# Performance work log

Hardware: AMD Instinct MI355X
Metric: run time of the kernel (lower is better)

The kernel has to match this reference:

```python
import jax, jax.numpy as jnp
import numpy as np

H, D_MODEL, D_K, D_V = 16, 1024, 64, 64
B, L = 4, 2048

def _linear_params(key, in_dim, out_dim):
    kw, kb = jax.random.split(key)
    bound = 1.0 / np.sqrt(in_dim)
    W = jax.random.uniform(kw, (out_dim, in_dim), jnp.float32, -bound, bound)
    b = jax.random.uniform(kb, (out_dim,), jnp.float32, -bound, bound)
    return W, b

def setup_inputs() -> dict:
    key = jax.random.key(0)
    ks = jax.random.split(key, 7)
    V = jax.random.normal(ks[0], (B, L, D_MODEL), jnp.float32)
    K = jax.random.normal(ks[1], (B, L, D_MODEL), jnp.float32)
    Q = jax.random.normal(ks[2], (B, L, D_MODEL), jnp.float32)
    Wv, bv = _linear_params(ks[3], D_MODEL, H * D_V)
    Wk, bk = _linear_params(ks[4], D_MODEL, H * D_K)
    Wq, bq = _linear_params(ks[5], D_MODEL, H * D_K)
    Wo, bo = _linear_params(ks[6], H * D_V, D_MODEL)
    return {"V": V, "K": K, "Q": Q, "Wv": Wv, "bv": bv, "Wk": Wk, "bk": bk,
            "Wq": Wq, "bq": bq, "Wo": Wo, "bo": bo}

def reference(V, K, Q, Wv, bv, Wk, bk, Wq, bq, Wo, bo):
    batch, len1, _ = V.shape
    len2 = Q.shape[1]
    # project and split heads: (b, l, h, d)
    v = (V @ Wv.T + bv).reshape(batch, len1, H, D_V)
    k = (K @ Wk.T + bk).reshape(batch, len1, H, D_K)
    q = (Q @ Wq.T + bq).reshape(batch, len2, H, D_K)
    scale = 1.0 / jnp.sqrt(jnp.asarray(D_K, q.dtype))
    # scores: (b, h, len2, len1)
    scores = jnp.einsum('bqhd,bkhd->bhqk', q, k) * scale
    attn = jax.nn.softmax(scores, axis=-1)
    out = jnp.einsum('bhqk,bkhd->bqhd', attn, v).reshape(batch, len2, H * D_V)
    return out @ Wo.T + bo
```

## Files before the change

### kernel.cpp

```cpp
#include <hip/hip_runtime.h>


typedef __bf16 bf16;
typedef __attribute__((ext_vector_type(8))) __bf16 bf16x8;
typedef __attribute__((ext_vector_type(4))) __bf16 bf16x4;
typedef __attribute__((ext_vector_type(4))) float f32x4;
typedef __attribute__((ext_vector_type(16))) float f32x16;

__global__ __launch_bounds__(256) void cvt_all(
    const float* __restrict__ Q, const float* __restrict__ K, const float* __restrict__ V,
    const float* __restrict__ Wq, const float* __restrict__ Wk,
    const float* __restrict__ Wv, const float* __restrict__ Wo,
    bf16* __restrict__ ws)
{
    int bid = blockIdx.x;
    const float* src;
    bf16* dst;
    int lb;
    if (bid < 4096)       { src = Q;  dst = ws;             lb = bid; }
    else if (bid < 8192)  { src = K;  dst = ws + 8388608;   lb = bid - 4096; }
    else if (bid < 12288) { src = V;  dst = ws + 16777216;  lb = bid - 8192; }
    else if (bid < 12800) { src = Wq; dst = ws + 25165824;  lb = bid - 12288; }
    else if (bid < 13312) { src = Wk; dst = ws + 26214400;  lb = bid - 12800; }
    else if (bid < 13824) { src = Wv; dst = ws + 27262976;  lb = bid - 13312; }
    else                  { src = Wo; dst = ws + 28311552;  lb = bid - 13824; }
    size_t i = ((size_t)lb * 256 + threadIdx.x) * 8;
    f32x4 a = *(const f32x4*)(src + i);
    f32x4 b = *(const f32x4*)(src + i + 4);
    bf16x8 o;
    o[0] = (bf16)a[0]; o[1] = (bf16)a[1]; o[2] = (bf16)a[2]; o[3] = (bf16)a[3];
    o[4] = (bf16)b[0]; o[5] = (bf16)b[1]; o[6] = (bf16)b[2]; o[7] = (bf16)b[3];
    *(bf16x8*)(dst + i) = o;
}

__device__ inline void gld_lds16(const void* g, void* l) {
    __builtin_amdgcn_global_load_lds((const __attribute__((address_space(1))) void*)g,
                                     (__attribute__((address_space(3))) void*)l, 16, 0, 0);
}

__global__ __launch_bounds__(512, 2) void proj_fused(
    const bf16* __restrict__ Xq, const bf16* __restrict__ Xk, const bf16* __restrict__ Xv,
    const bf16* __restrict__ Wqb, const bf16* __restrict__ Wkb, const bf16* __restrict__ Wvb,
    const float* __restrict__ bq, const float* __restrict__ bk, const float* __restrict__ bv,
    bf16* __restrict__ qw, bf16* __restrict__ kw, bf16* __restrict__ vtw)
{
    __shared__ bf16 lA[3][8192];
    __shared__ bf16 lB[3][8192];

    const int bid = blockIdx.x;
    const int xcd = bid & 7, idx = bid >> 3;
    const int chunk = idx >> 3, within = idx & 7;
    const int gc = xcd * 6 + chunk;
    const int z  = gc >> 4;
    const int mp = gc & 15;
    const int m0 = (mp * 2 + (within >> 2)) * 256;
    const int n0 = (within & 3) * 256;

    const bf16*  A    = z == 0 ? Xq  : (z == 1 ? Xk  : Xv);
    const bf16*  W    = z == 0 ? Wqb : (z == 1 ? Wkb : Wvb);
    const float* bias = z == 0 ? bq  : (z == 1 ? bk  : bv);
    bf16*        out  = z == 0 ? qw  : (z == 1 ? kw  : vtw);
    const float scale = z == 0 ? 0.18033688011112042f : 1.0f;

    const int tid  = threadIdx.x;
    const int wave = tid >> 6, lane = tid & 63;
    const int c = lane & 15, g = lane >> 4;
    const int wm = wave >> 2, wn = wave & 3;

    const int srow = lane >> 2;
    const int scol = ((lane & 3) ^ ((lane >> 3) & 3)) * 8;
    const int rsw  = (g ^ ((c >> 1) & 3)) * 8;

    f32x4 acc[8][4] = {};

#define SA(kt_, bb)                                                             \
    {                                                                           \
        _Pragma("unroll")                                                       \
        for (int j = 0; j < 2; ++j)                                             \
            gld_lds16(A + (size_t)(m0 + j * 128 + wave * 16 + srow) * 1024 +    \
                          (kt_) * 32 + scol,                                    \
                      &lA[bb][j * 4096 + wave * 512]);                          \
    }
#define SB(kt_, bb)                                                             \
    {                                                                           \
        _Pragma("unroll")                                                       \
        for (int j = 0; j < 2; ++j)                                             \
            gld_lds16(W + (size_t)(n0 + j * 128 + wave * 16 + srow) * 1024 +    \
                          (kt_) * 32 + scol,                                    \
                      &lB[bb][j * 4096 + wave * 512]);                          \
    }

    SA(0, 0); SB(0, 0);
    SA(1, 1); SB(1, 1);

    int buf = 0;
    for (int u = 0; u < 32; ++u) {
        if (u < 31) {
            asm volatile("s_waitcnt vmcnt(4)" ::: "memory");
        } else {
            asm volatile("s_waitcnt vmcnt(0)" ::: "memory");
        }
        __builtin_amdgcn_s_barrier();
        asm volatile("" ::: "memory");

        bf16x8 af[8], bfr[4];
#pragma unroll
        for (int m = 0; m < 8; ++m)
            af[m] = *(const bf16x8*)&lA[buf][(wm * 128 + m * 16 + c) * 32 + rsw];
#pragma unroll
        for (int n = 0; n < 4; ++n)
            bfr[n] = *(const bf16x8*)&lB[buf][(wn * 64 + n * 16 + c) * 32 + rsw];

        if (u + 2 < 32) {
            int nb = buf + 2; if (nb >= 3) nb -= 3;
            SA(u + 2, nb); SB(u + 2, nb);
        }

#pragma unroll
        for (int m = 0; m < 8; ++m)
#pragma unroll
            for (int n = 0; n < 4; ++n)
                acc[m][n] = __builtin_amdgcn_mfma_f32_16x16x32_bf16(af[m], bfr[n], acc[m][n], 0, 0, 0);

        buf = (buf == 2) ? 0 : buf + 1;
    }
#undef SA
#undef SB

#pragma unroll
    for (int m = 0; m < 8; ++m) {
#pragma unroll
        for (int n = 0; n < 4; ++n) {
            int col  = n0 + wn * 64 + n * 16 + c;
            float bb = bias[col];
#pragma unroll
            for (int r = 0; r < 4; ++r) {
                int row = m0 + wm * 128 + m * 16 + 4 * g + r;
                float v = (acc[m][n][r] + bb) * scale;
                int b = row >> 11, l = row & 2047, hh = col >> 6, d = col & 63;
                size_t base = (size_t)(b * 16 + hh) * 131072;
                if (z < 2) {
                    out[base + (l >> 5) * 2048 + (d >> 4) * 512 +
                        ((d >> 3) & 1) * 256 + (l & 31) * 8 + (d & 7)] = (bf16)v;
                } else {
                    out[base + (l >> 5) * 2048 + (d >> 5) * 1024 +
                        ((l >> 4) & 1) * 512 + ((l >> 3) & 1) * 256 +
                        (d & 31) * 8 + (l & 7)] = (bf16)v;
                }
            }
        }
    }
}

__global__ __launch_bounds__(256) void gemm_out(
    const bf16* __restrict__ A, const bf16* __restrict__ W,
    const float* __restrict__ bias, float* __restrict__ out)
{
    __shared__ bf16 lA[2][8192];
    __shared__ bf16 lB[2][8192];
    const int tid  = threadIdx.x;
    const int wave = tid >> 6, lane = tid & 63;
    const int c = lane & 15, g = lane >> 4;

    const int oid = blockIdx.y * 8 + blockIdx.x;
    const int nid = (oid & 7) * 64 + (oid >> 3);
    const int m0 = (nid >> 3) * 128, n0 = (nid & 7) * 128;

    const int wr = wave >> 1, wc = wave & 1;
    const int srow  = lane >> 3;
    const int scol8 = ((lane & 7) ^ srow) * 8;
    const int c7 = c & 7;

    f32x4 acc[4][4] = {};

#define OSTAGE(kt_, bb)                                                         \
    {                                                                           \
        _Pragma("unroll")                                                       \
        for (int i = 0; i < 4; ++i) {                                           \
            int ca = wave * 4 + i;                                              \
            int arow = ca * 8 + srow;                                           \
            gld_lds16(A + (size_t)(m0 + arow) * 1024 + (kt_) * 64 + scol8,      \
                      &lA[bb][ca * 512]);                                       \
            gld_lds16(W + (size_t)(n0 + arow) * 1024 + (kt_) * 64 + scol8,      \
                      &lB[bb][ca * 512]);                                       \
        }                                                                       \
    }

    OSTAGE(0, 0);
    OSTAGE(1, 1);

    for (int kt = 0; kt < 16; ++kt) {
        const int buf = kt & 1;
        if (kt < 15) {
            asm volatile("s_waitcnt vmcnt(8)" ::: "memory");
        } else {
            asm volatile("s_waitcnt vmcnt(0)" ::: "memory");
        }
        __builtin_amdgcn_s_barrier();
        asm volatile("" ::: "memory");

#pragma unroll
        for (int ks = 0; ks < 2; ++ks) {
            bf16x8 af[4], bfr[4];
#pragma unroll
            for (int m = 0; m < 4; ++m) {
                int r = wr * 64 + m * 16 + c;
                af[m] = *(const bf16x8*)&lA[buf][r * 64 + (((ks * 4 + g) ^ c7) * 8)];
            }
#pragma unroll
            for (int n = 0; n < 4; ++n) {
                int r = wc * 64 + n * 16 + c;
                bfr[n] = *(const bf16x8*)&lB[buf][r * 64 + (((ks * 4 + g) ^ c7) * 8)];
            }
#pragma unroll
            for (int m = 0; m < 4; ++m)
#pragma unroll
                for (int n = 0; n < 4; ++n)
                    acc[m][n] = __builtin_amdgcn_mfma_f32_16x16x32_bf16(af[m], bfr[n], acc[m][n], 0, 0, 0);
        }

        asm volatile("" ::: "memory");
        __builtin_amdgcn_s_barrier();
        asm volatile("" ::: "memory");
        if (kt + 2 < 16) OSTAGE(kt + 2, buf);
    }
#undef OSTAGE

#pragma unroll
    for (int m = 0; m < 4; ++m) {
#pragma unroll
        for (int n = 0; n < 4; ++n) {
            int col  = n0 + wc * 64 + n * 16 + c;
            float bb = bias[col];
#pragma unroll
            for (int r = 0; r < 4; ++r) {
                int row = m0 + wr * 64 + m * 16 + 4 * g + r;
                out[(size_t)row * 1024 + col] = acc[m][n][r] + bb;
            }
        }
    }
}

__device__ inline unsigned cvtpk(float lo, float hi) {
    unsigned r;
    asm("v_cvt_pk_bf16_f32 %0, %1, %2" : "=v"(r) : "v"(lo), "v"(hi));
    return r;
}
__device__ inline void pswap(unsigned &a, unsigned &b) {
    asm("v_permlane32_swap_b32 %0, %1" : "+v"(a), "+v"(b));
}

__global__ __launch_bounds__(512) void attn_kernel(
    const bf16* __restrict__ q, const bf16* __restrict__ k,
    const bf16* __restrict__ vt, bf16* __restrict__ O)
{
    __shared__ bf16 lkv[3][4096];
    const int tid  = threadIdx.x;
    const int wave = tid >> 6, lane = tid & 63;
    const int l31 = lane & 31, hi = lane >> 5;
    const int orig = blockIdx.x;
    const int swz  = (orig & 7) * 64 + (orig >> 3);
    const int bh = swz >> 3;
    const int q0 = (swz & 7) * 256 + wave * 32;
    const int laneoff = hi * 256 + l31 * 8;

    const bf16* qb = q  + (size_t)bh * 131072 + (q0 >> 5) * 2048 + laneoff;
    const bf16* kb = k  + (size_t)bh * 131072;
    const bf16* vb = vt + (size_t)bh * 131072;

    bf16x8 qf0 = *(const bf16x8*)(qb);
    bf16x8 qf1 = *(const bf16x8*)(qb + 512);
    bf16x8 qf2 = *(const bf16x8*)(qb + 1024);
    bf16x8 qf3 = *(const bf16x8*)(qb + 1536);

    const bf16* sg = (wave < 4) ? (kb + wave * 512 + lane * 8)
                                : (vb + (wave - 4) * 512 + lane * 8);
    const int   sl = (wave < 4) ? wave * 512 : 2048 + (wave - 4) * 512;

    bf16x8 ones;
#pragma unroll
    for (int i = 0; i < 8; ++i) ones[i] = (bf16)1.0f;

    f32x16 acc0 = {}, acc1 = {}, accS = {};

    gld_lds16(sg,        &lkv[0][sl]);
    gld_lds16(sg + 2048, &lkv[1][sl]);

    int cur = 0;
    for (int t = 0; t < 64; ++t) {
        if (t < 63) {
            asm volatile("s_waitcnt vmcnt(1)" ::: "memory");
        } else {
            asm volatile("s_waitcnt vmcnt(0)" ::: "memory");
        }
        __syncthreads();
        if (t + 2 < 64) {
            int nb = cur + 2; if (nb >= 3) nb -= 3;
            gld_lds16(sg + (size_t)(t + 2) * 2048, &lkv[nb][sl]);
        }

        const bf16* kl = &lkv[cur][laneoff];
        const bf16* vl = &lkv[cur][2048 + laneoff];
        bf16x8 kf0  = *(const bf16x8*)(kl);
        bf16x8 kf1  = *(const bf16x8*)(kl + 512);
        bf16x8 kf2  = *(const bf16x8*)(kl + 1024);
        bf16x8 kf3  = *(const bf16x8*)(kl + 1536);
        bf16x8 vf00 = *(const bf16x8*)(vl);
        bf16x8 vf01 = *(const bf16x8*)(vl + 512);
        bf16x8 vf10 = *(const bf16x8*)(vl + 1024);
        bf16x8 vf11 = *(const bf16x8*)(vl + 1536);

        f32x16 st = {};
        __builtin_amdgcn_s_setprio(1);
        st = __builtin_amdgcn_mfma_f32_32x32x16_bf16(kf0, qf0, st, 0, 0, 0);
        st = __builtin_amdgcn_mfma_f32_32x32x16_bf16(kf1, qf1, st, 0, 0, 0);
        st = __builtin_amdgcn_mfma_f32_32x32x16_bf16(kf2, qf2, st, 0, 0, 0);
        st = __builtin_amdgcn_mfma_f32_32x32x16_bf16(kf3, qf3, st, 0, 0, 0);
        __builtin_amdgcn_s_setprio(0);

#pragma unroll
        for (int r = 0; r < 16; ++r) st[r] = __builtin_amdgcn_exp2f(st[r]);

        unsigned u01 = cvtpk(st[0],  st[1]),  u23 = cvtpk(st[2],  st[3]);
        unsigned u45 = cvtpk(st[4],  st[5]),  u67 = cvtpk(st[6],  st[7]);
        unsigned u89 = cvtpk(st[8],  st[9]),  uAB = cvtpk(st[10], st[11]);
        unsigned uCD = cvtpk(st[12], st[13]), uEF = cvtpk(st[14], st[15]);
        pswap(u01, u45); pswap(u23, u67);
        pswap(u89, uCD); pswap(uAB, uEF);
        union { unsigned u[4]; bf16x8 v; } pf0, pf1;
        pf0.u[0] = u01; pf0.u[1] = u23; pf0.u[2] = u45; pf0.u[3] = u67;
        pf1.u[0] = u89; pf1.u[1] = uAB; pf1.u[2] = uCD; pf1.u[3] = uEF;

        __builtin_amdgcn_s_setprio(1);
        acc0 = __builtin_amdgcn_mfma_f32_32x32x16_bf16(vf00, pf0.v, acc0, 0, 0, 0);
        acc1 = __builtin_amdgcn_mfma_f32_32x32x16_bf16(vf10, pf0.v, acc1, 0, 0, 0);
        accS = __builtin_amdgcn_mfma_f32_32x32x16_bf16(ones, pf0.v, accS, 0, 0, 0);
        acc0 = __builtin_amdgcn_mfma_f32_32x32x16_bf16(vf01, pf1.v, acc0, 0, 0, 0);
        acc1 = __builtin_amdgcn_mfma_f32_32x32x16_bf16(vf11, pf1.v, acc1, 0, 0, 0);
        accS = __builtin_amdgcn_mfma_f32_32x32x16_bf16(ones, pf1.v, accS, 0, 0, 0);
        __builtin_amdgcn_s_setprio(0);

        cur = (cur == 2) ? 0 : cur + 1;
    }

    float inv = 1.0f / accS[0];
    int qg = q0 + l31;
    bf16* ob = O + ((size_t)(bh >> 4) * 2048 + qg) * 1024 + (size_t)(bh & 15) * 64;
#pragma unroll
    for (int rg = 0; rg < 4; ++rg) {
        bf16x4 w0, w1;
#pragma unroll
        for (int i = 0; i < 4; ++i) {
            w0[i] = (bf16)(acc0[rg * 4 + i] * inv);
            w1[i] = (bf16)(acc1[rg * 4 + i] * inv);
        }
        *(bf16x4*)(ob + 8 * rg + 4 * hi)      = w0;
        *(bf16x4*)(ob + 32 + 8 * rg + 4 * hi) = w1;
    }
}

extern "C" void kernel_launch(void* const* d_in, const int* in_sizes, int n_in,
                              void* d_out, int out_size, void* d_ws, size_t ws_size,
                              hipStream_t stream) {
    (void)in_sizes; (void)n_in; (void)out_size; (void)ws_size;
    const float* V  = (const float*)d_in[0];
    const float* K  = (const float*)d_in[1];
    const float* Q  = (const float*)d_in[2];
    const float* Wv = (const float*)d_in[3];
    const float* bv = (const float*)d_in[4];
    const float* Wk = (const float*)d_in[5];
    const float* bk = (const float*)d_in[6];
    const float* Wq = (const float*)d_in[7];
    const float* bq = (const float*)d_in[8];
    const float* Wo = (const float*)d_in[9];
    const float* bo = (const float*)d_in[10];

    char* ws = (char*)d_ws;
    const size_t MB = 1ull << 20;
    bf16* Xq  = (bf16*)(ws + 0);
    bf16* Xk  = (bf16*)(ws + 16 * MB);
    bf16* Xv  = (bf16*)(ws + 32 * MB);
    bf16* Wqb = (bf16*)(ws + 48 * MB);
    bf16* Wkb = (bf16*)(ws + 50 * MB);
    bf16* Wvb = (bf16*)(ws + 52 * MB);
    bf16* Wob = (bf16*)(ws + 54 * MB);
    bf16* qw  = (bf16*)(ws + 56 * MB);
    bf16* kw  = (bf16*)(ws + 72 * MB);
    bf16* vtw = (bf16*)(ws + 88 * MB);
    bf16* Ow  = (bf16*)(ws + 0);

    cvt_all<<<14336, 256, 0, stream>>>(Q, K, V, Wq, Wk, Wv, Wo, (bf16*)ws);

    proj_fused<<<384, 512, 0, stream>>>(
        Xq, Xk, Xv, Wqb, Wkb, Wvb, bq, bk, bv, qw, kw, vtw);

    attn_kernel<<<512, 512, 0, stream>>>(qw, kw, vtw, Ow);

    gemm_out<<<dim3(8, 64), 256, 0, stream>>>(Ow, Wob, bo, (float*)d_out);
}
```

Measured before the change: 203.4 us.

## Double-buffer projection GEMM LDS and compute softmax row sums with VALU

The projection GEMM drops from a triple-buffered LDS ring to two buffers. The next tile is now issued after a second barrier that follows the MFMAs, which cuts LDS use and may let more blocks fit per CU, at the price of an extra barrier per k-step. In attention, the row-sum normalizer no longer runs as two extra MFMAs against a ones vector. It is accumulated in VALU adds and combined with a cross-lane shuffle, and the setprio hints are removed. This trades matrix-core work for vector ALU work and may change overlap between the two.

```diff
diff --git a/kernel.cpp b/kernel.cpp
--- a/kernel.cpp
+++ b/kernel.cpp
@@ -44,8 +44,8 @@
     const float* __restrict__ bq, const float* __restrict__ bk, const float* __restrict__ bv,
     bf16* __restrict__ qw, bf16* __restrict__ kw, bf16* __restrict__ vtw)
 {
-    __shared__ bf16 lA[3][8192];
-    __shared__ bf16 lB[3][8192];
+    __shared__ bf16 lA[2][8192];
+    __shared__ bf16 lB[2][8192];
 
     const int bid = blockIdx.x;
     const int xcd = bid & 7, idx = bid >> 3;
@@ -73,29 +73,25 @@
 
     f32x4 acc[8][4] = {};
 
-#define SA(kt_, bb)                                                             \
+#define SAB(kt_, bb)                                                            \
     {                                                                           \
         _Pragma("unroll")                                                       \
-        for (int j = 0; j < 2; ++j)                                             \
+        for (int j = 0; j < 2; ++j) {                                           \
             gld_lds16(A + (size_t)(m0 + j * 128 + wave * 16 + srow) * 1024 +    \
                           (kt_) * 32 + scol,                                    \
                       &lA[bb][j * 4096 + wave * 512]);                          \
-    }
-#define SB(kt_, bb)                                                             \
-    {                                                                           \
-        _Pragma("unroll")                                                       \
-        for (int j = 0; j < 2; ++j)                                             \
             gld_lds16(W + (size_t)(n0 + j * 128 + wave * 16 + srow) * 1024 +    \
                           (kt_) * 32 + scol,                                    \
                       &lB[bb][j * 4096 + wave * 512]);                          \
-    }
-
-    SA(0, 0); SB(0, 0);
-    SA(1, 1); SB(1, 1);
-
-    int buf = 0;
-    for (int u = 0; u < 32; ++u) {
-        if (u < 31) {
+        }                                                                       \
+    }
+
+    SAB(0, 0);
+    SAB(1, 1);
+
+    for (int kt = 0; kt < 32; ++kt) {
+        const int buf = kt & 1;
+        if (kt < 31) {
             asm volatile("s_waitcnt vmcnt(4)" ::: "memory");
         } else {
             asm volatile("s_waitcnt vmcnt(0)" ::: "memory");
@@ -111,21 +107,18 @@
         for (int n = 0; n < 4; ++n)
             bfr[n] = *(const bf16x8*)&lB[buf][(wn * 64 + n * 16 + c) * 32 + rsw];
 
-        if (u + 2 < 32) {
-            int nb = buf + 2; if (nb >= 3) nb -= 3;
-            SA(u + 2, nb); SB(u + 2, nb);
-        }
-
 #pragma unroll
         for (int m = 0; m < 8; ++m)
 #pragma unroll
             for (int n = 0; n < 4; ++n)
                 acc[m][n] = __builtin_amdgcn_mfma_f32_16x16x32_bf16(af[m], bfr[n], acc[m][n], 0, 0, 0);
 
-        buf = (buf == 2) ? 0 : buf + 1;
-    }
-#undef SA
-#undef SB
+        asm volatile("" ::: "memory");
+        __builtin_amdgcn_s_barrier();
+        asm volatile("" ::: "memory");
+        if (kt + 2 < 32) SAB(kt + 2, buf);
+    }
+#undef SAB
 
 #pragma unroll
     for (int m = 0; m < 8; ++m) {
@@ -277,11 +270,8 @@
                                 : (vb + (wave - 4) * 512 + lane * 8);
     const int   sl = (wave < 4) ? wave * 512 : 2048 + (wave - 4) * 512;
 
-    bf16x8 ones;
-#pragma unroll
-    for (int i = 0; i < 8; ++i) ones[i] = (bf16)1.0f;
-
-    f32x16 acc0 = {}, acc1 = {}, accS = {};
+    f32x16 acc0 = {}, acc1 = {};
+    float lsum = 0.f;
 
     gld_lds16(sg,        &lkv[0][sl]);
     gld_lds16(sg + 2048, &lkv[1][sl]);
@@ -311,15 +301,19 @@
         bf16x8 vf11 = *(const bf16x8*)(vl + 1536);
 
         f32x16 st = {};
-        __builtin_amdgcn_s_setprio(1);
         st = __builtin_amdgcn_mfma_f32_32x32x16_bf16(kf0, qf0, st, 0, 0, 0);
         st = __builtin_amdgcn_mfma_f32_32x32x16_bf16(kf1, qf1, st, 0, 0, 0);
         st = __builtin_amdgcn_mfma_f32_32x32x16_bf16(kf2, qf2, st, 0, 0, 0);
         st = __builtin_amdgcn_mfma_f32_32x32x16_bf16(kf3, qf3, st, 0, 0, 0);
-        __builtin_amdgcn_s_setprio(0);
 
 #pragma unroll
         for (int r = 0; r < 16; ++r) st[r] = __builtin_amdgcn_exp2f(st[r]);
+
+        float s0 = (st[0] + st[1]) + (st[2] + st[3]);
+        float s1 = (st[4] + st[5]) + (st[6] + st[7]);
+        float s2 = (st[8] + st[9]) + (st[10] + st[11]);
+        float s3 = (st[12] + st[13]) + (st[14] + st[15]);
+        lsum += (s0 + s1) + (s2 + s3);
 
         unsigned u01 = cvtpk(st[0],  st[1]),  u23 = cvtpk(st[2],  st[3]);
         unsigned u45 = cvtpk(st[4],  st[5]),  u67 = cvtpk(st[6],  st[7]);
@@ -331,19 +325,16 @@
         pf0.u[0] = u01; pf0.u[1] = u23; pf0.u[2] = u45; pf0.u[3] = u67;
         pf1.u[0] = u89; pf1.u[1] = uAB; pf1.u[2] = uCD; pf1.u[3] = uEF;
 
-        __builtin_amdgcn_s_setprio(1);
         acc0 = __builtin_amdgcn_mfma_f32_32x32x16_bf16(vf00, pf0.v, acc0, 0, 0, 0);
         acc1 = __builtin_amdgcn_mfma_f32_32x32x16_bf16(vf10, pf0.v, acc1, 0, 0, 0);
-        accS = __builtin_amdgcn_mfma_f32_32x32x16_bf16(ones, pf0.v, accS, 0, 0, 0);
         acc0 = __builtin_amdgcn_mfma_f32_32x32x16_bf16(vf01, pf1.v, acc0, 0, 0, 0);
         acc1 = __builtin_amdgcn_mfma_f32_32x32x16_bf16(vf11, pf1.v, acc1, 0, 0, 0);
-        accS = __builtin_amdgcn_mfma_f32_32x32x16_bf16(ones, pf1.v, accS, 0, 0, 0);
-        __builtin_amdgcn_s_setprio(0);
 
         cur = (cur == 2) ? 0 : cur + 1;
     }
 
-    float inv = 1.0f / accS[0];
+    lsum += __shfl_xor(lsum, 32);
+    float inv = 1.0f / lsum;
     int qg = q0 + l31;
     bf16* ob = O + ((size_t)(bh >> 4) * 2048 + qg) * 1024 + (size_t)(bh & 15) * 64;
 #pragma unroll
```

Result: slower. 217.0 us (+6.7%).
